# Performance work log

Hardware: AMD Instinct MI355X
Metric: run time of the kernel (lower is better)

Reference implementation:

```python
import jax, jax.numpy as jnp
import numpy as np

B, C, N, H, W = 8, 128, 16, 56, 56
HID, OUT = 128, 128


def conv1x1(x, w, b):
    # 1x1x1 Conv3d == channel-mixing GEMM. x: [B,Cin,N,H,W], w: [Cout,Cin], b: [Cout]
    return jnp.einsum('oc,bcnhw->bonhw', w, x) + b[None, :, None, None, None]


def setup_inputs() -> dict:
    key = jax.random.key(0)
    ks = jax.random.split(key, 9)
    s = 0.02
    return {
        'x': jax.random.normal(ks[0], (B, C, N, H, W), dtype=jnp.float32),
        'w_q': jax.random.normal(ks[1], (HID, C), dtype=jnp.float32) * s,
        'b_q': jax.random.normal(ks[2], (HID,), dtype=jnp.float32) * s,
        'w_k': jax.random.normal(ks[3], (HID, C), dtype=jnp.float32) * s,
        'b_k': jax.random.normal(ks[4], (HID,), dtype=jnp.float32) * s,
        'w_v': jax.random.normal(ks[5], (HID, C), dtype=jnp.float32) * s,
        'b_v': jax.random.normal(ks[6], (HID,), dtype=jnp.float32) * s,
        'w_o': jax.random.normal(ks[7], (OUT, HID), dtype=jnp.float32) * s,
        'b_o': jax.random.normal(ks[8], (OUT,), dtype=jnp.float32) * s,
    }


def reference(x, w_q, b_q, w_k, b_k, w_v, b_v, w_o, b_o):
    Bsz, Cc, Nn, Hh, Ww = x.shape
    L = Nn * Hh * Ww
    q = conv1x1(x, w_q, b_q).reshape(Bsz, -1, L)   # [B, hid, L]
    k = conv1x1(x, w_k, b_k).reshape(Bsz, -1, L)   # [B, hid, L]
    v = conv1x1(x, w_v, b_v).reshape(Bsz, -1, L)   # [B, hid, L]
    # NOTE: attention is over CHANNELS (hid x hid), since k was transposed to [B, L, hid]
    attn = jax.nn.softmax(jnp.einsum('bql,bkl->bqk', q, k), axis=-1)  # [B, hid, hid]
    feats = jnp.einsum('bqk,bkl->bql', attn, v).reshape(Bsz, -1, Nn, Hh, Ww)
    out = conv1x1(feats, w_o, b_o) + x             # residual requires out_dim == in_dim
    return jnp.mean(out, axis=2)                   # mean over N (depth) -> [B, out, H, W]
```

## Files before the change

### kernel.cpp

```cpp
#include <hip/hip_runtime.h>
#include <hip/hip_bf16.h>
#include <cstdint>

#define BB   8
#define CCH  128
#define NND  16
#define HWD  3136
#define LLT  50176
#define HWB  32
#define NHB  98
#define K3WB 64
#define K3NB 49

#define OFF_SP  0
#define OFF_RP  12845056
#define OFF_S   12945408
#define OFF_M   13076480
#define OFF_Q   13207552
#define OFF_AV  13338624
#define OFF_CV  13339648

typedef __attribute__((ext_vector_type(8)))  short bf16x8;
typedef __attribute__((ext_vector_type(16))) float f32x16;

__device__ __forceinline__ uint32_t fbits(float f){ union{float f;uint32_t u;}v; v.f=f; return v.u; }
__device__ __forceinline__ float bitsf(uint32_t u){ union{uint32_t u;float f;}v; v.u=u; return v.f; }

#define MFMA32(a,b,c) __builtin_amdgcn_mfma_f32_32x32x16_bf16((a),(b),(c),0,0,0)

__global__ __launch_bounds__(256,3) void k1_gram(const float* __restrict__ x,
    float* __restrict__ Sp, float* __restrict__ rp, float* __restrict__ Y)
{
  __shared__ __align__(16) short lds_h[2][4*128*8];
  __shared__ __align__(16) short lds_l[2][4*128*8];
  const int b   = blockIdx.x / NHB;
  const int hb  = blockIdx.x % NHB;
  const int hw0 = hb * HWB;
  const int tid = threadIdx.x;
  const int lane = tid & 63, w = tid >> 6;
  const int wr = w >> 1, wc = w & 1;
  const int rr  = tid >> 1, h = tid & 1;
  const float* xb = x + (size_t)b*CCH*LLT + (size_t)rr*LLT + hw0 + 16*h;

  f32x16 acc[2][2];
  #pragma unroll
  for(int ai=0;ai<2;ai++)
    #pragma unroll
    for(int bi=0;bi<2;bi++)
      #pragma unroll
      for(int e=0;e<16;e++) acc[ai][bi][e] = 0.f;
  float yac[16];
  #pragma unroll
  for(int i=0;i<16;i++) yac[i]=0.f;

  float4 v[4];
  #pragma unroll
  for(int u=0;u<4;u++) v[u] = *(const float4*)(xb + 4*u);

#define SPLIT(bufi)                                                         \
  {                                                                         \
    _Pragma("unroll")                                                       \
    for(int c2=0;c2<2;c2++){                                                \
      int hwd_[4], lwd_[4];                                                 \
      _Pragma("unroll")                                                     \
      for(int q=0;q<2;q++){                                                 \
        const int u = 2*c2+q;                                               \
        const float x0=v[u].x, x1=v[u].y, x2=v[u].z, x3=v[u].w;             \
        const uint32_t a0=fbits(x0),a1=fbits(x1),a2=fbits(x2),a3=fbits(x3); \
        hwd_[2*q+0] = __builtin_amdgcn_perm(a1, a0, 0x07060302u);           \
        hwd_[2*q+1] = __builtin_amdgcn_perm(a3, a2, 0x07060302u);           \
        const float l0 = x0 - bitsf(a0&0xFFFF0000u);                        \
        const float l1 = x1 - bitsf(a1&0xFFFF0000u);                        \
        const float l2 = x2 - bitsf(a2&0xFFFF0000u);                        \
        const float l3 = x3 - bitsf(a3&0xFFFF0000u);                        \
        lwd_[2*q+0] = __builtin_amdgcn_perm(fbits(l1), fbits(l0), 0x07060302u); \
        lwd_[2*q+1] = __builtin_amdgcn_perm(fbits(l3), fbits(l2), 0x07060302u); \
        yac[4*u+0]+=x0; yac[4*u+1]+=x1; yac[4*u+2]+=x2; yac[4*u+3]+=x3;     \
      }                                                                     \
      const int kc = 2*h + c2;                                              \
      *(int4*)&lds_h[bufi][(kc*128 + rr)*8] = make_int4(hwd_[0],hwd_[1],hwd_[2],hwd_[3]); \
      *(int4*)&lds_l[bufi][(kc*128 + rr)*8] = make_int4(lwd_[0],lwd_[1],lwd_[2],lwd_[3]); \
    }                                                                       \
  }

  SPLIT(0);
  __syncthreads();
  #pragma unroll
  for(int u=0;u<4;u++) v[u] = *(const float4*)(xb + HWD + 4*u);

  for(int n=0;n<NND;n++){
    const int cur = n & 1;
    #pragma unroll
    for(int ks=0;ks<2;ks++){
      const int kc = 2*ks + (lane>>5);
      const int rbase = (kc*128 + (lane&31))*8;
      const bf16x8 a0h = *(const bf16x8*)&lds_h[cur][rbase + (64*wr    )*8];
      const bf16x8 a0l = *(const bf16x8*)&lds_l[cur][rbase + (64*wr    )*8];
      const bf16x8 a1h = *(const bf16x8*)&lds_h[cur][rbase + (64*wr+32)*8];
      const bf16x8 a1l = *(const bf16x8*)&lds_l[cur][rbase + (64*wr+32)*8];
      const bf16x8 b0h = *(const bf16x8*)&lds_h[cur][rbase + (64*wc    )*8];
      const bf16x8 b0l = *(const bf16x8*)&lds_l[cur][rbase + (64*wc    )*8];
      const bf16x8 b1h = *(const bf16x8*)&lds_h[cur][rbase + (64*wc+32)*8];
      const bf16x8 b1l = *(const bf16x8*)&lds_l[cur][rbase + (64*wc+32)*8];
      acc[0][0] = MFMA32(a0h, b0h, acc[0][0]);
      acc[0][0] = MFMA32(a0h, b0l, acc[0][0]);
      acc[0][0] = MFMA32(a0l, b0h, acc[0][0]);
      acc[0][1] = MFMA32(a0h, b1h, acc[0][1]);
      acc[0][1] = MFMA32(a0h, b1l, acc[0][1]);
      acc[0][1] = MFMA32(a0l, b1h, acc[0][1]);
      acc[1][0] = MFMA32(a1h, b0h, acc[1][0]);
      acc[1][0] = MFMA32(a1h, b0l, acc[1][0]);
      acc[1][0] = MFMA32(a1l, b0h, acc[1][0]);
      acc[1][1] = MFMA32(a1h, b1h, acc[1][1]);
      acc[1][1] = MFMA32(a1h, b1l, acc[1][1]);
      acc[1][1] = MFMA32(a1l, b1h, acc[1][1]);
    }
    if(n+1 < NND){
      SPLIT(cur^1);
      __syncthreads();
      if(n+2 < NND){
        #pragma unroll
        for(int u=0;u<4;u++) v[u] = *(const float4*)(xb + (size_t)(n+2)*HWD + 4*u);
      }
    }
  }
#undef SPLIT

  #pragma unroll
  for(int u=0;u<4;u++){
    float4 o4 = make_float4(yac[4*u]*0.0625f, yac[4*u+1]*0.0625f,
                            yac[4*u+2]*0.0625f, yac[4*u+3]*0.0625f);
    *(float4*)(Y + ((size_t)b*CCH + rr)*HWD + hw0 + 16*h + 4*u) = o4;
  }
  float p = 0.f;
  #pragma unroll
  for(int i=0;i<16;i++) p += yac[i];
  p += __shfl_xor(p, 1);
  if(h==0) rp[(size_t)(b*NHB+hb)*CCH + rr] = p;

  float* Sb = Sp + (size_t)(b*NHB+hb)*CCH*CCH;
  const int col = lane & 31, roff = 4*(lane>>5);
  #pragma unroll
  for(int ai=0;ai<2;ai++)
    #pragma unroll
    for(int bi=0;bi<2;bi++)
      #pragma unroll
      for(int reg=0;reg<16;reg++){
        const int row = 64*wr + 32*ai + roff + (reg&3) + 8*(reg>>2);
        Sb[(size_t)row*CCH + 64*wc + 32*bi + col] = acc[ai][bi][reg];
      }
}

__global__ __launch_bounds__(256) void k1r(const float* __restrict__ Sp,
                                           float* __restrict__ S)
{
  const int b  = blockIdx.x >> 4;
  const int ch = blockIdx.x & 15;
  const int i  = ch*1024 + threadIdx.x*4;
  const float* p = Sp + (size_t)b*NHB*CCH*CCH + i;
  float4 s = make_float4(0.f,0.f,0.f,0.f);
  for(int hb=0;hb<NHB;hb++){
    float4 v = *(const float4*)(p + (size_t)hb*CCH*CCH);
    s.x+=v.x; s.y+=v.y; s.z+=v.z; s.w+=v.w;
  }
  *(float4*)(S + (size_t)b*CCH*CCH + i) = s;
}

__global__ __launch_bounds__(256) void k2ab(const float* __restrict__ S, const float* __restrict__ rp,
    const float* __restrict__ wq, const float* __restrict__ bq,
    const float* __restrict__ wk, const float* __restrict__ bk,
    const float* __restrict__ wv, const float* __restrict__ bv,
    float* __restrict__ M, float* __restrict__ av)
{
  __shared__ __align__(16) float t1[16][132];
  __shared__ float rb_s[CCH];
  __shared__ float wrk_s[CCH];
  __shared__ float wrq_s[16];
  const int b   = blockIdx.x >> 3;
  const int r0  = (blockIdx.x & 7) * 16;
  const int tid = threadIdx.x;
  const float* Sb = S + (size_t)b*CCH*CCH;

  if(tid < CCH){
    float s = 0.f;
    const float* rpb = rp + (size_t)b*NHB*CCH + tid;
    for(int hb=0;hb<NHB;hb++) s += rpb[hb*CCH];
    rb_s[tid] = s;
  }
  __syncthreads();

  if(tid < CCH){
    float s = 0.f;
    for(int m=0;m<CCH;m++) s += wk[(size_t)tid*CCH+m]*rb_s[m];
    wrk_s[tid] = s;
  } else if(tid < CCH+16){
    const int rr2 = tid - CCH;
    float s = 0.f;
    for(int m=0;m<CCH;m++) s += wq[(size_t)(r0+rr2)*CCH+m]*rb_s[m];
    wrq_s[rr2] = s;
  }

  const int rr = tid >> 4;
  const int c0 = (tid & 15) * 8;
  {
    float a8[8] = {0,0,0,0,0,0,0,0};
    const float* wqr = wq + (size_t)(r0+rr)*CCH;
    for(int m4=0;m4<32;m4++){
      float4 w4 = *(const float4*)(wqr + 4*m4);
      const float wl[4] = {w4.x,w4.y,w4.z,w4.w};
      #pragma unroll
      for(int mm=0;mm<4;mm++){
        const int m = 4*m4+mm;
        const float w = wl[mm];
        float4 s0 = *(const float4*)(Sb + (size_t)m*CCH + c0);
        float4 s1 = *(const float4*)(Sb + (size_t)m*CCH + c0 + 4);
        a8[0]=fmaf(w,s0.x,a8[0]); a8[1]=fmaf(w,s0.y,a8[1]);
        a8[2]=fmaf(w,s0.z,a8[2]); a8[3]=fmaf(w,s0.w,a8[3]);
        a8[4]=fmaf(w,s1.x,a8[4]); a8[5]=fmaf(w,s1.y,a8[5]);
        a8[6]=fmaf(w,s1.z,a8[6]); a8[7]=fmaf(w,s1.w,a8[7]);
      }
    }
    #pragma unroll
    for(int j=0;j<8;j++) t1[rr][c0+j] = a8[j];
  }
  __syncthreads();

  const int j0 = c0;
  float g[8] = {0,0,0,0,0,0,0,0};
  for(int c4=0;c4<32;c4++){
    float4 tv = *(const float4*)(&t1[rr][4*c4]);
    #pragma unroll
    for(int jj=0;jj<8;jj++){
      float4 w4 = *(const float4*)(wk + (size_t)(j0+jj)*CCH + 4*c4);
      g[jj]=fmaf(tv.x,w4.x,g[jj]); g[jj]=fmaf(tv.y,w4.y,g[jj]);
      g[jj]=fmaf(tv.z,w4.z,g[jj]); g[jj]=fmaf(tv.w,w4.w,g[jj]);
    }
  }
  const float bqr  = bq[r0+rr];
  const float wrqr = wrq_s[rr];
  #pragma unroll
  for(int jj=0;jj<8;jj++)
    g[jj] += wrqr*bk[j0+jj] + bqr*wrk_s[j0+jj] + (float)LLT*bqr*bk[j0+jj];

  float mx = g[0];
  #pragma unroll
  for(int jj=1;jj<8;jj++) mx = fmaxf(mx, g[jj]);
  #pragma unroll
  for(int s=1;s<16;s<<=1) mx = fmaxf(mx, __shfl_xor(mx, s, 16));
  float ex[8], sum=0.f;
  #pragma unroll
  for(int jj=0;jj<8;jj++){ ex[jj] = expf(g[jj]-mx); sum += ex[jj]; }
  #pragma unroll
  for(int s=1;s<16;s<<=1) sum += __shfl_xor(sum, s, 16);
  const float inv = 1.0f/sum;

  float pa = 0.f;
  #pragma unroll
  for(int jj=0;jj<8;jj++) pa += ex[jj]*inv*bv[j0+jj];
  #pragma unroll
  for(int s=1;s<16;s<<=1) pa += __shfl_xor(pa, s, 16);
  if((tid&15)==0) av[b*CCH + r0+rr] = pa;

  __syncthreads();
  #pragma unroll
  for(int jj=0;jj<8;jj++) t1[rr][j0+jj] = ex[jj]*inv;
  __syncthreads();

  {
    float a8[8] = {0,0,0,0,0,0,0,0};
    for(int k4=0;k4<32;k4++){
      float4 a4 = *(const float4*)(&t1[rr][4*k4]);
      const float al[4] = {a4.x,a4.y,a4.z,a4.w};
      #pragma unroll
      for(int kk=0;kk<4;kk++){
        const int k = 4*k4+kk;
        const float wgt = al[kk];
        float4 v0 = *(const float4*)(wv + (size_t)k*CCH + c0);
        float4 v1 = *(const float4*)(wv + (size_t)k*CCH + c0 + 4);
        a8[0]=fmaf(wgt,v0.x,a8[0]); a8[1]=fmaf(wgt,v0.y,a8[1]);
        a8[2]=fmaf(wgt,v0.z,a8[2]); a8[3]=fmaf(wgt,v0.w,a8[3]);
        a8[4]=fmaf(wgt,v1.x,a8[4]); a8[5]=fmaf(wgt,v1.y,a8[5]);
        a8[6]=fmaf(wgt,v1.z,a8[6]); a8[7]=fmaf(wgt,v1.w,a8[7]);
      }
    }
    float* Mr = M + ((size_t)b*CCH + r0+rr)*CCH + c0;
    *(float4*)(Mr  ) = make_float4(a8[0],a8[1],a8[2],a8[3]);
    *(float4*)(Mr+4) = make_float4(a8[4],a8[5],a8[6],a8[7]);
  }
}

__global__ __launch_bounds__(256) void k2c(const float* __restrict__ M,
    const float* __restrict__ wo, const float* __restrict__ bo,
    const float* __restrict__ av, float* __restrict__ Q, float* __restrict__ cv)
{
  const int b  = blockIdx.x >> 3;
  const int o0 = (blockIdx.x & 7)*16;
  const int tid = threadIdx.x;
  const int rr = tid>>4, c0 = (tid&15)*8;
  const int o  = o0 + rr;
  const float* wor = wo + (size_t)o*CCH;
  const float* Mb  = M + (size_t)b*CCH*CCH;
  float a8[8] = {0,0,0,0,0,0,0,0};
  for(int m4=0;m4<32;m4++){
    float4 w4 = *(const float4*)(wor + 4*m4);
    const float wl[4] = {w4.x,w4.y,w4.z,w4.w};
    #pragma unroll
    for(int mm=0;mm<4;mm++){
      const int m = 4*m4+mm;
      const float w = wl[mm];
      float4 v0 = *(const float4*)(Mb + (size_t)m*CCH + c0);
      float4 v1 = *(const float4*)(Mb + (size_t)m*CCH + c0 + 4);
      a8[0]=fmaf(w,v0.x,a8[0]); a8[1]=fmaf(w,v0.y,a8[1]);
      a8[2]=fmaf(w,v0.z,a8[2]); a8[3]=fmaf(w,v0.w,a8[3]);
      a8[4]=fmaf(w,v1.x,a8[4]); a8[5]=fmaf(w,v1.y,a8[5]);
      a8[6]=fmaf(w,v1.z,a8[6]); a8[7]=fmaf(w,v1.w,a8[7]);
    }
  }
  #pragma unroll
  for(int j=0;j<8;j++) if(o == c0+j) a8[j] += 1.0f;
  float* Qr = Q + ((size_t)b*CCH + o)*CCH + c0;
  *(float4*)(Qr  ) = make_float4(a8[0],a8[1],a8[2],a8[3]);
  *(float4*)(Qr+4) = make_float4(a8[4],a8[5],a8[6],a8[7]);

  if(tid < 16){
    const int oo = o0 + tid;
    float s = 0.f;
    for(int m=0;m<CCH;m++) s += wo[(size_t)oo*CCH+m]*av[b*CCH+m];
    cv[b*CCH + oo] = s + bo[oo];
  }
}

__global__ __launch_bounds__(256,2) void k3(const float* __restrict__ Q,
    const float* __restrict__ cv, float* __restrict__ out)
{
  __shared__ __align__(16) float4 qs[4096];
  const int b   = blockIdx.x / K3NB;
  const int hb  = blockIdx.x % K3NB;
  const int hw0 = hb * K3WB;
  const int tid = threadIdx.x;

  const float4* Qg = (const float4*)(Q + (size_t)b*CCH*CCH);
  #pragma unroll
  for(int it=0; it<16; it++){
    const int idx = it*256 + tid;
    const int row = idx >> 5, ch = idx & 31;
    qs[(row<<5) | (ch ^ (row>>3))] = Qg[idx];
  }
  __syncthreads();

  const int tx = tid & 15, ty = tid >> 4;
  const int o0 = tx*8;
  const int hg = ty*4;
  float acc[8][4];
  #pragma unroll
  for(int i=0;i<8;i++){ acc[i][0]=0.f; acc[i][1]=0.f; acc[i][2]=0.f; acc[i][3]=0.f; }

  const float* Yb = out + (size_t)b*CCH*HWD + hw0 + hg;
  for(int c4=0;c4<32;c4++){
    float4 yv[4];
    #pragma unroll
    for(int mm=0;mm<4;mm++) yv[mm] = *(const float4*)(Yb + (size_t)(4*c4+mm)*HWD);
    #pragma unroll
    for(int i=0;i<8;i++){
      const int row = o0 + i;
      const float4 q4 = qs[(row<<5) | (c4 ^ tx)];
      const float ql[4] = {q4.x,q4.y,q4.z,q4.w};
      #pragma unroll
      for(int mm=0;mm<4;mm++){
        acc[i][0]=fmaf(ql[mm],yv[mm].x,acc[i][0]);
        acc[i][1]=fmaf(ql[mm],yv[mm].y,acc[i][1]);
        acc[i][2]=fmaf(ql[mm],yv[mm].z,acc[i][2]);
        acc[i][3]=fmaf(ql[mm],yv[mm].w,acc[i][3]);
      }
    }
  }
  __syncthreads();
  #pragma unroll
  for(int i=0;i<8;i++){
    const float c = cv[b*CCH + o0+i];
    float4 o4 = make_float4(acc[i][0]+c, acc[i][1]+c, acc[i][2]+c, acc[i][3]+c);
    *(float4*)(out + ((size_t)b*CCH + o0+i)*HWD + hw0 + hg) = o4;
  }
}

extern "C" void kernel_launch(void* const* d_in, const int* in_sizes, int n_in,
                              void* d_out, int out_size, void* d_ws, size_t ws_size,
                              hipStream_t stream) {
  const float* x  = (const float*)d_in[0];
  const float* wq = (const float*)d_in[1];
  const float* bq = (const float*)d_in[2];
  const float* wk = (const float*)d_in[3];
  const float* bk = (const float*)d_in[4];
  const float* wv = (const float*)d_in[5];
  const float* bv = (const float*)d_in[6];
  const float* wo = (const float*)d_in[7];
  const float* bo = (const float*)d_in[8];
  float* out = (float*)d_out;
  float* ws  = (float*)d_ws;

  k1_gram<<<BB*NHB, 256, 0, stream>>>(x, ws+OFF_SP, ws+OFF_RP, out);
  k1r<<<128, 256, 0, stream>>>(ws+OFF_SP, ws+OFF_S);
  k2ab<<<64, 256, 0, stream>>>(ws+OFF_S, ws+OFF_RP, wq, bq, wk, bk, wv, bv,
                               ws+OFF_M, ws+OFF_AV);
  k2c<<<64, 256, 0, stream>>>(ws+OFF_M, wo, bo, ws+OFF_AV, ws+OFF_Q, ws+OFF_CV);
  k3<<<BB*K3NB, 256, 0, stream>>>(ws+OFF_Q, ws+OFF_CV, out);
}
```

Baseline: 173.6 us.

## Remap gram-kernel loads to 8 threads per row and pad LDS rows

The gram kernel's global load mapping changes so that 8 consecutive threads read one 128-byte contiguous channel row segment, instead of 2 threads each reading 64 bytes. This should give better-coalesced transactions. The LDS staging arrays are padded from 128 to 129 rows per k-chunk to reduce bank conflicts on the narrower int2 stores and the MFMA operand reads. The row-sum reduction now uses an 8-lane shuffle tree, and launch bounds are raised from 3 to 4 blocks per CU, which may limit registers and risk spilling.

```diff
diff --git a/kernel.cpp b/kernel.cpp
--- a/kernel.cpp
+++ b/kernel.cpp
@@ -28,19 +28,21 @@
 
 #define MFMA32(a,b,c) __builtin_amdgcn_mfma_f32_32x32x16_bf16((a),(b),(c),0,0,0)
 
-__global__ __launch_bounds__(256,3) void k1_gram(const float* __restrict__ x,
+__global__ __launch_bounds__(256,4) void k1_gram(const float* __restrict__ x,
     float* __restrict__ Sp, float* __restrict__ rp, float* __restrict__ Y)
 {
-  __shared__ __align__(16) short lds_h[2][4*128*8];
-  __shared__ __align__(16) short lds_l[2][4*128*8];
+  __shared__ __align__(16) short lds_h[2][4*129*8];
+  __shared__ __align__(16) short lds_l[2][4*129*8];
   const int b   = blockIdx.x / NHB;
   const int hb  = blockIdx.x % NHB;
   const int hw0 = hb * HWB;
   const int tid = threadIdx.x;
   const int lane = tid & 63, w = tid >> 6;
   const int wr = w >> 1, wc = w & 1;
-  const int rr  = tid >> 1, h = tid & 1;
-  const float* xb = x + (size_t)b*CCH*LLT + (size_t)rr*LLT + hw0 + 16*h;
+  const int cr = tid >> 3;
+  const int p  = tid & 7;
+  const int kc = p >> 1, hf = p & 1;
+  const float* xb = x + (size_t)b*CCH*LLT + (size_t)cr*LLT + hw0 + 4*p;
 
   f32x16 acc[2][2];
   #pragma unroll
@@ -55,45 +57,41 @@
 
   float4 v[4];
   #pragma unroll
-  for(int u=0;u<4;u++) v[u] = *(const float4*)(xb + 4*u);
+  for(int j=0;j<4;j++) v[j] = *(const float4*)(xb + (size_t)(32*j)*LLT);
 
 #define SPLIT(bufi)                                                         \
   {                                                                         \
     _Pragma("unroll")                                                       \
-    for(int c2=0;c2<2;c2++){                                                \
-      int hwd_[4], lwd_[4];                                                 \
-      _Pragma("unroll")                                                     \
-      for(int q=0;q<2;q++){                                                 \
-        const int u = 2*c2+q;                                               \
-        const float x0=v[u].x, x1=v[u].y, x2=v[u].z, x3=v[u].w;             \
-        const uint32_t a0=fbits(x0),a1=fbits(x1),a2=fbits(x2),a3=fbits(x3); \
-        hwd_[2*q+0] = __builtin_amdgcn_perm(a1, a0, 0x07060302u);           \
-        hwd_[2*q+1] = __builtin_amdgcn_perm(a3, a2, 0x07060302u);           \
-        const float l0 = x0 - bitsf(a0&0xFFFF0000u);                        \
-        const float l1 = x1 - bitsf(a1&0xFFFF0000u);                        \
-        const float l2 = x2 - bitsf(a2&0xFFFF0000u);                        \
-        const float l3 = x3 - bitsf(a3&0xFFFF0000u);                        \
-        lwd_[2*q+0] = __builtin_amdgcn_perm(fbits(l1), fbits(l0), 0x07060302u); \
-        lwd_[2*q+1] = __builtin_amdgcn_perm(fbits(l3), fbits(l2), 0x07060302u); \
-        yac[4*u+0]+=x0; yac[4*u+1]+=x1; yac[4*u+2]+=x2; yac[4*u+3]+=x3;     \
-      }                                                                     \
-      const int kc = 2*h + c2;                                              \
-      *(int4*)&lds_h[bufi][(kc*128 + rr)*8] = make_int4(hwd_[0],hwd_[1],hwd_[2],hwd_[3]); \
-      *(int4*)&lds_l[bufi][(kc*128 + rr)*8] = make_int4(lwd_[0],lwd_[1],lwd_[2],lwd_[3]); \
+    for(int j=0;j<4;j++){                                                   \
+      const int c = 32*j + cr;                                              \
+      const float x0=v[j].x, x1=v[j].y, x2=v[j].z, x3=v[j].w;               \
+      const uint32_t a0=fbits(x0),a1=fbits(x1),a2=fbits(x2),a3=fbits(x3);   \
+      const int h0 = __builtin_amdgcn_perm(a1, a0, 0x07060302u);            \
+      const int h1 = __builtin_amdgcn_perm(a3, a2, 0x07060302u);            \
+      const float l0 = x0 - bitsf(a0&0xFFFF0000u);                          \
+      const float l1 = x1 - bitsf(a1&0xFFFF0000u);                          \
+      const float l2 = x2 - bitsf(a2&0xFFFF0000u);                          \
+      const float l3 = x3 - bitsf(a3&0xFFFF0000u);                          \
+      const int g0 = __builtin_amdgcn_perm(fbits(l1), fbits(l0), 0x07060302u); \
+      const int g1 = __builtin_amdgcn_perm(fbits(l3), fbits(l2), 0x07060302u); \
+      const int sa = (kc*129 + c)*8 + 4*hf;                                 \
+      *(int2*)&lds_h[bufi][sa] = make_int2(h0,h1);                          \
+      *(int2*)&lds_l[bufi][sa] = make_int2(g0,g1);                          \
+      yac[4*j+0]+=x0; yac[4*j+1]+=x1; yac[4*j+2]+=x2; yac[4*j+3]+=x3;       \
     }                                                                       \
   }
 
   SPLIT(0);
   __syncthreads();
   #pragma unroll
-  for(int u=0;u<4;u++) v[u] = *(const float4*)(xb + HWD + 4*u);
+  for(int j=0;j<4;j++) v[j] = *(const float4*)(xb + (size_t)(32*j)*LLT + HWD);
 
   for(int n=0;n<NND;n++){
     const int cur = n & 1;
     #pragma unroll
     for(int ks=0;ks<2;ks++){
-      const int kc = 2*ks + (lane>>5);
-      const int rbase = (kc*128 + (lane&31))*8;
+      const int kk = 2*ks + (lane>>5);
+      const int rbase = (kk*129 + (lane&31))*8;
       const bf16x8 a0h = *(const bf16x8*)&lds_h[cur][rbase + (64*wr    )*8];
       const bf16x8 a0l = *(const bf16x8*)&lds_l[cur][rbase + (64*wr    )*8];
       const bf16x8 a1h = *(const bf16x8*)&lds_h[cur][rbase + (64*wr+32)*8];
@@ -120,23 +118,26 @@
       __syncthreads();
       if(n+2 < NND){
         #pragma unroll
-        for(int u=0;u<4;u++) v[u] = *(const float4*)(xb + (size_t)(n+2)*HWD + 4*u);
+        for(int j=0;j<4;j++)
+          v[j] = *(const float4*)(xb + (size_t)(32*j)*LLT + (size_t)(n+2)*HWD);
       }
     }
   }
 #undef SPLIT
 
   #pragma unroll
-  for(int u=0;u<4;u++){
-    float4 o4 = make_float4(yac[4*u]*0.0625f, yac[4*u+1]*0.0625f,
-                            yac[4*u+2]*0.0625f, yac[4*u+3]*0.0625f);
-    *(float4*)(Y + ((size_t)b*CCH + rr)*HWD + hw0 + 16*h + 4*u) = o4;
-  }
-  float p = 0.f;
-  #pragma unroll
-  for(int i=0;i<16;i++) p += yac[i];
-  p += __shfl_xor(p, 1);
-  if(h==0) rp[(size_t)(b*NHB+hb)*CCH + rr] = p;
+  for(int j=0;j<4;j++){
+    float4 o4 = make_float4(yac[4*j]*0.0625f, yac[4*j+1]*0.0625f,
+                            yac[4*j+2]*0.0625f, yac[4*j+3]*0.0625f);
+    *(float4*)(Y + ((size_t)b*CCH + 32*j + cr)*HWD + hw0 + 4*p) = o4;
+  }
+  #pragma unroll
+  for(int j=0;j<4;j++){
+    float s = yac[4*j]+yac[4*j+1]+yac[4*j+2]+yac[4*j+3];
+    #pragma unroll
+    for(int st=1;st<8;st<<=1) s += __shfl_xor(s, st, 8);
+    if(p==0) rp[(size_t)(b*NHB+hb)*CCH + 32*j + cr] = s;
+  }
 
   float* Sb = Sp + (size_t)(b*NHB+hb)*CCH*CCH;
   const int col = lane & 31, roff = 4*(lane>>5);
```

New measurement: 165.5 us. 4.7% less time.
